# Optimization experiments

Hardware: AMD Instinct MI355X
Metric: run time of the kernel (lower is better)

Reference implementation:

```python
import jax, jax.numpy as jnp
import numpy as np

DIM = 512        # token feature dim
HID = 1024       # expert hidden dim (dim * 2)
E = 16           # num_experts
N = 8192         # num tokens
TOPK = 2         # experts active per token (routing sparsity)


def setup_inputs() -> dict:
    key = jax.random.key(0)
    k_x, k_s, k_w1, k_w2 = jax.random.split(key, 4)
    x = jax.random.normal(k_x, (N, DIM), dtype=jnp.float32)
    # sparse routing scores: top-2 experts per token get nonzero score, rest 0
    scores = jax.random.uniform(k_s, (N, E), dtype=jnp.float32)
    vals, idx = jax.lax.top_k(scores, TOPK)
    routing_tensor = jnp.zeros((N, E), jnp.float32).at[jnp.arange(N)[:, None], idx].set(vals)
    # per-expert MLP params (depth=2, bias=True): Linear(DIM->HID), GELU, Linear(HID->DIM)
    W1 = jax.random.normal(k_w1, (E, DIM, HID), dtype=jnp.float32) * (1.0 / np.sqrt(DIM))
    b1 = jnp.zeros((E, HID), jnp.float32)
    W2 = jax.random.normal(k_w2, (E, HID, DIM), dtype=jnp.float32) * (1.0 / np.sqrt(HID))
    b2 = jnp.zeros((E, DIM), jnp.float32)
    return {"x": x, "routing_tensor": routing_tensor, "W1": W1, "b1": b1, "W2": W2, "b2": b2}


def reference(x, routing_tensor, W1, b1, W2, b2):
    # out[n] = sum_e routing[n,e] * MLP_e(x[n]); rows with score 0 contribute 0,
    # which is exactly the original mask-gather / scatter-add semantics.
    h = jax.nn.gelu(jnp.einsum('nd,edh->enh', x, W1) + b1[:, None, :], approximate=False)
    y = jnp.einsum('enh,ehd->end', h, W2) + b2[:, None, :]  # [E, N, DIM]
    return jnp.einsum('end,ne->nd', y, routing_tensor)       # combine weighted by scores
```

## Files before the change

### kernel.cpp

```cpp
#include <hip/hip_runtime.h>
#include <hip/hip_bf16.h>

#define NTOK 8192
#define DIM 512
#define HID 1024
#define NE 16
#define CAP 1280
#define MT 20

typedef __attribute__((ext_vector_type(8))) short short8;
typedef __attribute__((ext_vector_type(4))) float f32x4;

static __device__ __forceinline__ unsigned short f2bf(float f) {
    __hip_bfloat16 h = __float2bfloat16(f);
    return __builtin_bit_cast(unsigned short, h);
}

static __device__ __forceinline__ void gl_lds16(const unsigned short* g, unsigned short* l) {
    __builtin_amdgcn_global_load_lds(
        (const __attribute__((address_space(1))) unsigned int*)g,
        (__attribute__((address_space(3))) unsigned int*)l, 16, 0, 0);
}

static __device__ __forceinline__ float gelu_f(float v) {
    float u = v * (0.7978845608f + 0.0356774081f * v * v);
    return v / (1.0f + __expf(-2.0f * u));
}

__global__ __launch_bounds__(256) void prep(const float* __restrict__ W1,
                                            const float* __restrict__ W2,
                                            unsigned short* __restrict__ w1t,
                                            unsigned short* __restrict__ w2t,
                                            const float* __restrict__ routing,
                                            int* __restrict__ cnt,
                                            int* __restrict__ sidx,
                                            float* __restrict__ wtb) {
    int b = blockIdx.x;
    int t = threadIdx.x;
    if (b < 4096) {
        __shared__ float tile[64][65];
        const float* src; unsigned short* dst; int R, C, bx, by;
        if (b < 2048) {
            int e = b >> 7, rem = b & 127; bx = rem & 15; by = rem >> 4;
            R = DIM; C = HID;
            src = W1 + (size_t)e * R * C; dst = w1t + (size_t)e * R * C;
        } else {
            int bb = b - 2048;
            int e = bb >> 7, rem = bb & 127; bx = rem & 7; by = rem >> 3;
            R = HID; C = DIM;
            src = W2 + (size_t)e * R * C; dst = w2t + (size_t)e * R * C;
        }
        int c0 = bx * 64, r0 = by * 64;
        int tx = t & 15, ty = t >> 4;
        #pragma unroll
        for (int i = 0; i < 4; i++) {
            float4 v = *(const float4*)(src + (size_t)(r0 + ty + i * 16) * C + c0 + tx * 4);
            tile[ty + i * 16][tx * 4 + 0] = v.x;
            tile[ty + i * 16][tx * 4 + 1] = v.y;
            tile[ty + i * 16][tx * 4 + 2] = v.z;
            tile[ty + i * 16][tx * 4 + 3] = v.w;
        }
        __syncthreads();
        #pragma unroll
        for (int i = 0; i < 4; i++) {
            int dr = ty + i * 16;
            ushort4 o;
            o.x = f2bf(tile[tx * 4 + 0][dr]);
            o.y = f2bf(tile[tx * 4 + 1][dr]);
            o.z = f2bf(tile[tx * 4 + 2][dr]);
            o.w = f2bf(tile[tx * 4 + 3][dr]);
            *(ushort4*)(dst + (size_t)(c0 + dr) * R + r0 + tx * 4) = o;
        }
    } else {
        __shared__ int lcnt[NE], lbase[NE];
        int n = (b - 4096) * 256 + t;
        if (t < NE) lcnt[t] = 0;
        __syncthreads();
        int mye[2]; float myw[2]; int mypos[2]; int slot = 0;
        #pragma unroll
        for (int e = 0; e < NE; e++) {
            float r = routing[n * NE + e];
            if (r != 0.0f && slot < 2) {
                mye[slot] = e; myw[slot] = r;
                mypos[slot] = atomicAdd(&lcnt[e], 1);
                slot++;
            }
        }
        __syncthreads();
        if (t < NE) lbase[t] = atomicAdd(&cnt[t], lcnt[t]);
        __syncthreads();
        for (int s = 0; s < slot; s++) {
            int e = mye[s];
            int p = lbase[e] + mypos[s];
            if (p < CAP) { sidx[e * CAP + p] = n * 2 + s; wtb[e * CAP + p] = myw[s]; }
        }
    }
}

__global__ void gather_x(const float* __restrict__ x, const int* __restrict__ cnt,
                         const int* __restrict__ sidx, unsigned short* __restrict__ xg) {
    int b = blockIdx.x;
    int e = b / CAP, row = b - e * CAP;
    int t = threadIdx.x;
    int c = cnt[e]; c = c > CAP ? CAP : c;
    ushort4 o;
    if (row < c) {
        int n = sidx[b] >> 1;
        float4 v = ((const float4*)(x + (size_t)n * DIM))[t];
        o.x = f2bf(v.x); o.y = f2bf(v.y); o.z = f2bf(v.z); o.w = f2bf(v.w);
    } else {
        o.x = 0; o.y = 0; o.z = 0; o.w = 0;
    }
    ((ushort4*)(xg + (size_t)b * DIM))[t] = o;
}

template <int K>
__device__ __forceinline__ void mfma_main64(const unsigned short* __restrict__ A,
                                            const unsigned short* __restrict__ B,
                                            unsigned short* As, unsigned short* Bs,
                                            f32x4 acc[2][4]) {
    int t = threadIdx.x;
    int wave = t >> 6, lane = t & 63;
    int wm = wave >> 1, wn = wave & 1;
    int quad = lane >> 4, l16 = lane & 15;
    int lr = lane >> 3;
    int col = (lane & 7) << 3;
    for (int kc = 0; kc < K; kc += 64) {
        __syncthreads();
        #pragma unroll
        for (int j = 0; j < 2; j++) {
            int rb = wave * 16 + j * 8;
            gl_lds16(A + (size_t)(rb + lr) * K + kc + col, As + rb * 64);
        }
        #pragma unroll
        for (int j = 0; j < 4; j++) {
            int rb = wave * 32 + j * 8;
            gl_lds16(B + (size_t)(rb + lr) * K + kc + col, Bs + rb * 64);
        }
        __syncthreads();
        #pragma unroll
        for (int kk = 0; kk < 64; kk += 32) {
            short8 av[2], bv[4];
            #pragma unroll
            for (int mt = 0; mt < 2; mt++)
                av[mt] = *(const short8*)(&As[(wm * 32 + mt * 16 + l16) * 64 + kk + quad * 8]);
            #pragma unroll
            for (int nt = 0; nt < 4; nt++)
                bv[nt] = *(const short8*)(&Bs[(wn * 64 + nt * 16 + l16) * 64 + kk + quad * 8]);
            #pragma unroll
            for (int mt = 0; mt < 2; mt++)
                #pragma unroll
                for (int nt = 0; nt < 4; nt++)
                    acc[mt][nt] = __builtin_amdgcn_mfma_f32_16x16x32_bf16(
                        av[mt], bv[nt], acc[mt][nt], 0, 0, 0);
        }
    }
}


__global__ __launch_bounds__(256, 5) void gemm1_gelu(
    const unsigned short* __restrict__ xg, const unsigned short* __restrict__ w1t,
    const float* __restrict__ b1, const int* __restrict__ cnt,
    unsigned short* __restrict__ hbuf) {
    __shared__ __align__(16) unsigned short As[64 * 64];
    __shared__ __align__(16) unsigned short Bs[128 * 64];
    int L = blockIdx.x;
    int cc = L & 7, n = (L >> 3) & 7, g = L >> 6;
    int pi = cc + (g << 3);
    int e = pi / MT, m = pi % MT;
    int c = cnt[e]; c = c > CAP ? CAP : c;
    int m0 = m * 64;
    if (m0 >= c) return;
    int n0 = n * 128;
    const unsigned short* A = xg + ((size_t)e * CAP + m0) * DIM;
    const unsigned short* B = w1t + ((size_t)e * HID + n0) * DIM;
    f32x4 z = {0.f, 0.f, 0.f, 0.f};
    f32x4 acc[2][4];
    #pragma unroll
    for (int mt = 0; mt < 2; mt++)
        #pragma unroll
        for (int nt = 0; nt < 4; nt++) acc[mt][nt] = z;
    mfma_main64<DIM>(A, B, As, Bs, acc);
    int t = threadIdx.x;
    int wave = t >> 6, lane = t & 63;
    int wm = wave >> 1, wn = wave & 1, quad = lane >> 4, l16 = lane & 15;
    #pragma unroll
    for (int nt = 0; nt < 4; nt++) {
        int gn = n0 + wn * 64 + nt * 16 + l16;
        float bias = b1[e * HID + gn];
        #pragma unroll
        for (int mt = 0; mt < 2; mt++) {
            #pragma unroll
            for (int r = 0; r < 4; r++) {
                int gm = m0 + wm * 32 + mt * 16 + quad * 4 + r;
                float v = acc[mt][nt][r] + bias;
                hbuf[((size_t)e * CAP + gm) * HID + gn] = f2bf(gelu_f(v));
            }
        }
    }
}

__global__ __launch_bounds__(256, 5) void gemm2_store(
    const unsigned short* __restrict__ hbuf, const unsigned short* __restrict__ w2t,
    const float* __restrict__ b2, const int* __restrict__ cnt,
    const int* __restrict__ sidx, const float* __restrict__ wtb,
    float* __restrict__ ybuf) {
    __shared__ __align__(16) unsigned short As[64 * 64];
    __shared__ __align__(16) unsigned short Bs[128 * 64];
    int L = blockIdx.x;
    int cc = L & 7, n = (L >> 3) & 3, g = L >> 5;
    int pi = cc + (g << 3);
    int e = pi / MT, m = pi % MT;
    int c = cnt[e]; c = c > CAP ? CAP : c;
    int m0 = m * 64;
    if (m0 >= c) return;
    int n0 = n * 128;
    const unsigned short* A = hbuf + ((size_t)e * CAP + m0) * HID;
    const unsigned short* B = w2t + ((size_t)e * DIM + n0) * HID;
    f32x4 z = {0.f, 0.f, 0.f, 0.f};
    f32x4 acc[2][4];
    #pragma unroll
    for (int mt = 0; mt < 2; mt++)
        #pragma unroll
        for (int nt = 0; nt < 4; nt++) acc[mt][nt] = z;
    mfma_main64<HID>(A, B, As, Bs, acc);
    int t = threadIdx.x;
    int wave = t >> 6, lane = t & 63;
    int wm = wave >> 1, wn = wave & 1, quad = lane >> 4, l16 = lane & 15;
    #pragma unroll
    for (int mt = 0; mt < 2; mt++) {
        #pragma unroll
        for (int r = 0; r < 4; r++) {
            int gm = m0 + wm * 32 + mt * 16 + quad * 4 + r;
            if (gm < c) {
                int si = sidx[e * CAP + gm];
                float wgt = wtb[e * CAP + gm];
                float* yrow = ybuf + (size_t)si * DIM;
                #pragma unroll
                for (int nt = 0; nt < 4; nt++) {
                    int gn = n0 + wn * 64 + nt * 16 + l16;
                    yrow[gn] = wgt * (acc[mt][nt][r] + b2[e * DIM + gn]);
                }
            }
        }
    }
}

__global__ void combine(const float* __restrict__ yb, float* __restrict__ out) {
    int i = blockIdx.x * 256 + threadIdx.x;
    int n = i >> 7, d4 = i & 127;
    float4 a = ((const float4*)(yb + (size_t)(2 * n) * DIM))[d4];
    float4 b = ((const float4*)(yb + (size_t)(2 * n + 1) * DIM))[d4];
    float4 o;
    o.x = a.x + b.x; o.y = a.y + b.y; o.z = a.z + b.z; o.w = a.w + b.w;
    ((float4*)(out + (size_t)n * DIM))[d4] = o;
}

extern "C" void kernel_launch(void* const* d_in, const int* in_sizes, int n_in,
                              void* d_out, int out_size, void* d_ws, size_t ws_size,
                              hipStream_t stream) {
    const float* x       = (const float*)d_in[0];
    const float* routing = (const float*)d_in[1];
    const float* W1      = (const float*)d_in[2];
    const float* b1      = (const float*)d_in[3];
    const float* W2      = (const float*)d_in[4];
    const float* b2      = (const float*)d_in[5];
    float* out = (float*)d_out;

    char* w = (char*)d_ws;
    int*   cnt  = (int*)w;
    int*   sidx = (int*)(w + 256);
    float* wtb  = (float*)(w + 256 + NE * CAP * 4);
    char* base = w + 256 + NE * CAP * 8;
    unsigned short* xg  = (unsigned short*)base;
    unsigned short* hb  = xg + (size_t)NE * CAP * DIM;
    unsigned short* w1t = hb + (size_t)NE * CAP * HID;
    unsigned short* w2t = w1t + (size_t)NE * HID * DIM;
    float* ybuf = (float*)(w2t + (size_t)NE * DIM * HID);

    hipMemsetAsync(cnt, 0, 256, stream);

    prep<<<4096 + NTOK / 256, 256, 0, stream>>>(W1, W2, w1t, w2t, routing, cnt, sidx, wtb);
    gather_x<<<NE * CAP, 128, 0, stream>>>(x, cnt, sidx, xg);

    gemm1_gelu<<<8 * MT * NE, 256, 0, stream>>>(xg, w1t, b1, cnt, hb);
    gemm2_store<<<4 * MT * NE, 256, 0, stream>>>(hb, w2t, b2, cnt, sidx, wtb, ybuf);
    combine<<<(NTOK * DIM / 4) / 256, 256, 0, stream>>>(ybuf, out);
}
```

Measured before the change: 224.2 us.

## Fuse token gather and bf16 conversion into gemm1 A-tile load; widen transpose stores

Drops the separate gather_x kernel and its bf16 xg buffer. gemm1 now reads routed token rows of x directly through sidx, converts them to bf16 in registers and writes them to LDS. The weight transpose also now stores 8 bf16 values per thread instead of 4. This saves a kernel launch and a full write and read of the gathered activations. In exchange, each of the 8 N-tile blocks re-reads and re-converts the fp32 rows, and the synchronous A-tile loads may stall the MFMA loop.

Measured after the change: 253.7 us. 13.2% more time.

```diff
diff --git a/kernel.cpp b/kernel.cpp
--- a/kernel.cpp
+++ b/kernel.cpp
@@ -9,6 +9,7 @@
 #define MT 20
 
 typedef __attribute__((ext_vector_type(8))) short short8;
+typedef __attribute__((ext_vector_type(8))) unsigned short us8;
 typedef __attribute__((ext_vector_type(4))) float f32x4;
 
 static __device__ __forceinline__ unsigned short f2bf(float f) {
@@ -61,15 +62,15 @@
             tile[ty + i * 16][tx * 4 + 3] = v.w;
         }
         __syncthreads();
-        #pragma unroll
-        for (int i = 0; i < 4; i++) {
-            int dr = ty + i * 16;
-            ushort4 o;
-            o.x = f2bf(tile[tx * 4 + 0][dr]);
-            o.y = f2bf(tile[tx * 4 + 1][dr]);
-            o.z = f2bf(tile[tx * 4 + 2][dr]);
-            o.w = f2bf(tile[tx * 4 + 3][dr]);
-            *(ushort4*)(dst + (size_t)(c0 + dr) * R + r0 + tx * 4) = o;
+        int seg = t & 7;
+        #pragma unroll
+        for (int i = 0; i < 2; i++) {
+            int dr = (t >> 3) + i * 32;
+            us8 o;
+            #pragma unroll
+            for (int j = 0; j < 8; j++)
+                o[j] = f2bf(tile[seg * 8 + j][dr]);
+            *(us8*)(dst + (size_t)(c0 + dr) * R + r0 + seg * 8) = o;
         }
     } else {
         __shared__ int lcnt[NE], lbase[NE];
@@ -97,21 +98,93 @@
     }
 }
 
-__global__ void gather_x(const float* __restrict__ x, const int* __restrict__ cnt,
-                         const int* __restrict__ sidx, unsigned short* __restrict__ xg) {
-    int b = blockIdx.x;
-    int e = b / CAP, row = b - e * CAP;
+
+__global__ __launch_bounds__(256, 5) void gemm1_gelu(
+    const float* __restrict__ x, const unsigned short* __restrict__ w1t,
+    const float* __restrict__ b1, const int* __restrict__ cnt,
+    const int* __restrict__ sidx, unsigned short* __restrict__ hbuf) {
+    __shared__ __align__(16) unsigned short As[64 * 64];
+    __shared__ __align__(16) unsigned short Bs[128 * 64];
+    int L = blockIdx.x;
+    int cc = L & 7, n = (L >> 3) & 7, g = L >> 6;
+    int pi = cc + (g << 3);
+    int e = pi / MT, m = pi % MT;
+    int c = cnt[e]; c = c > CAP ? CAP : c;
+    int m0 = m * 64;
+    if (m0 >= c) return;
+    int n0 = n * 128;
+    const unsigned short* B = w1t + ((size_t)e * HID + n0) * DIM;
+
     int t = threadIdx.x;
-    int c = cnt[e]; c = c > CAP ? CAP : c;
-    ushort4 o;
-    if (row < c) {
-        int n = sidx[b] >> 1;
-        float4 v = ((const float4*)(x + (size_t)n * DIM))[t];
-        o.x = f2bf(v.x); o.y = f2bf(v.y); o.z = f2bf(v.z); o.w = f2bf(v.w);
-    } else {
-        o.x = 0; o.y = 0; o.z = 0; o.w = 0;
-    }
-    ((ushort4*)(xg + (size_t)b * DIM))[t] = o;
+    int wave = t >> 6, lane = t & 63;
+    int wm = wave >> 1, wn = wave & 1;
+    int quad = lane >> 4, l16 = lane & 15;
+    int lr = lane >> 3;
+    int colB = (lane & 7) << 3;
+
+    int rA = t >> 4, cA = (t & 15) * 4;
+    const float* xrow[4];
+    #pragma unroll
+    for (int p = 0; p < 4; p++) {
+        int gr = m0 + rA + p * 16;
+        int si = (gr < c) ? sidx[e * CAP + gr] : -1;
+        xrow[p] = (si >= 0) ? (x + (size_t)(si >> 1) * DIM) : nullptr;
+    }
+
+    f32x4 z = {0.f, 0.f, 0.f, 0.f};
+    f32x4 acc[2][4];
+    #pragma unroll
+    for (int mt = 0; mt < 2; mt++)
+        #pragma unroll
+        for (int nt = 0; nt < 4; nt++) acc[mt][nt] = z;
+
+    for (int kc = 0; kc < DIM; kc += 64) {
+        __syncthreads();
+        #pragma unroll
+        for (int j = 0; j < 4; j++) {
+            int rb = wave * 32 + j * 8;
+            gl_lds16(B + (size_t)(rb + lr) * DIM + kc + colB, Bs + rb * 64);
+        }
+        #pragma unroll
+        for (int p = 0; p < 4; p++) {
+            float4 v = xrow[p] ? *(const float4*)(xrow[p] + kc + cA)
+                               : make_float4(0.f, 0.f, 0.f, 0.f);
+            ushort4 o;
+            o.x = f2bf(v.x); o.y = f2bf(v.y); o.z = f2bf(v.z); o.w = f2bf(v.w);
+            *(ushort4*)(&As[(rA + p * 16) * 64 + cA]) = o;
+        }
+        __syncthreads();
+        #pragma unroll
+        for (int kk = 0; kk < 64; kk += 32) {
+            short8 av[2], bv[4];
+            #pragma unroll
+            for (int mt = 0; mt < 2; mt++)
+                av[mt] = *(const short8*)(&As[(wm * 32 + mt * 16 + l16) * 64 + kk + quad * 8]);
+            #pragma unroll
+            for (int nt = 0; nt < 4; nt++)
+                bv[nt] = *(const short8*)(&Bs[(wn * 64 + nt * 16 + l16) * 64 + kk + quad * 8]);
+            #pragma unroll
+            for (int mt = 0; mt < 2; mt++)
+                #pragma unroll
+                for (int nt = 0; nt < 4; nt++)
+                    acc[mt][nt] = __builtin_amdgcn_mfma_f32_16x16x32_bf16(
+                        av[mt], bv[nt], acc[mt][nt], 0, 0, 0);
+        }
+    }
+    #pragma unroll
+    for (int nt = 0; nt < 4; nt++) {
+        int gn = n0 + wn * 64 + nt * 16 + l16;
+        float bias = b1[e * HID + gn];
+        #pragma unroll
+        for (int mt = 0; mt < 2; mt++) {
+            #pragma unroll
+            for (int r = 0; r < 4; r++) {
+                int gm = m0 + wm * 32 + mt * 16 + quad * 4 + r;
+                float v = acc[mt][nt][r] + bias;
+                hbuf[((size_t)e * CAP + gm) * HID + gn] = f2bf(gelu_f(v));
+            }
+        }
+    }
 }
 
 template <int K>
@@ -153,49 +226,6 @@
                 for (int nt = 0; nt < 4; nt++)
                     acc[mt][nt] = __builtin_amdgcn_mfma_f32_16x16x32_bf16(
                         av[mt], bv[nt], acc[mt][nt], 0, 0, 0);
-        }
-    }
-}
-
-
-__global__ __launch_bounds__(256, 5) void gemm1_gelu(
-    const unsigned short* __restrict__ xg, const unsigned short* __restrict__ w1t,
-    const float* __restrict__ b1, const int* __restrict__ cnt,
-    unsigned short* __restrict__ hbuf) {
-    __shared__ __align__(16) unsigned short As[64 * 64];
-    __shared__ __align__(16) unsigned short Bs[128 * 64];
-    int L = blockIdx.x;
-    int cc = L & 7, n = (L >> 3) & 7, g = L >> 6;
-    int pi = cc + (g << 3);
-    int e = pi / MT, m = pi % MT;
-    int c = cnt[e]; c = c > CAP ? CAP : c;
-    int m0 = m * 64;
-    if (m0 >= c) return;
-    int n0 = n * 128;
-    const unsigned short* A = xg + ((size_t)e * CAP + m0) * DIM;
-    const unsigned short* B = w1t + ((size_t)e * HID + n0) * DIM;
-    f32x4 z = {0.f, 0.f, 0.f, 0.f};
-    f32x4 acc[2][4];
-    #pragma unroll
-    for (int mt = 0; mt < 2; mt++)
-        #pragma unroll
-        for (int nt = 0; nt < 4; nt++) acc[mt][nt] = z;
-    mfma_main64<DIM>(A, B, As, Bs, acc);
-    int t = threadIdx.x;
-    int wave = t >> 6, lane = t & 63;
-    int wm = wave >> 1, wn = wave & 1, quad = lane >> 4, l16 = lane & 15;
-    #pragma unroll
-    for (int nt = 0; nt < 4; nt++) {
-        int gn = n0 + wn * 64 + nt * 16 + l16;
-        float bias = b1[e * HID + gn];
-        #pragma unroll
-        for (int mt = 0; mt < 2; mt++) {
-            #pragma unroll
-            for (int r = 0; r < 4; r++) {
-                int gm = m0 + wm * 32 + mt * 16 + quad * 4 + r;
-                float v = acc[mt][nt][r] + bias;
-                hbuf[((size_t)e * CAP + gm) * HID + gn] = f2bf(gelu_f(v));
-            }
         }
     }
 }
@@ -272,8 +302,7 @@
     int*   sidx = (int*)(w + 256);
     float* wtb  = (float*)(w + 256 + NE * CAP * 4);
     char* base = w + 256 + NE * CAP * 8;
-    unsigned short* xg  = (unsigned short*)base;
-    unsigned short* hb  = xg + (size_t)NE * CAP * DIM;
+    unsigned short* hb  = (unsigned short*)base;
     unsigned short* w1t = hb + (size_t)NE * CAP * HID;
     unsigned short* w2t = w1t + (size_t)NE * HID * DIM;
     float* ybuf = (float*)(w2t + (size_t)NE * DIM * HID);
@@ -281,9 +310,8 @@
     hipMemsetAsync(cnt, 0, 256, stream);
 
     prep<<<4096 + NTOK / 256, 256, 0, stream>>>(W1, W2, w1t, w2t, routing, cnt, sidx, wtb);
-    gather_x<<<NE * CAP, 128, 0, stream>>>(x, cnt, sidx, xg);
-
-    gemm1_gelu<<<8 * MT * NE, 256, 0, stream>>>(xg, w1t, b1, cnt, hb);
+
+    gemm1_gelu<<<8 * MT * NE, 256, 0, stream>>>(x, w1t, b1, cnt, sidx, hb);
     gemm2_store<<<4 * MT * NE, 256, 0, stream>>>(hb, w2t, b2, cnt, sidx, wtb, ybuf);
     combine<<<(NTOK * DIM / 4) / 256, 256, 0, stream>>>(ybuf, out);
 }
```

## Split routing into own kernel and fuse x gather into weight-transpose kernel

Applied to the files above, without the earlier changes.

Routing/counting moves into a small standalone kernel, and the x gather/bf16 conversion is merged into the weight transpose kernel as extra blocks. Each gather block now handles four rows with 16-byte stores, and the transpose writes 8 bf16 values per store instead of 4. The goal is to cut the tiny 128-thread gather blocks, let the gather overlap with the weight conversion, and widen global stores. It adds a launch for the routing kernel, and the transpose now reads LDS with a different access pattern.

Result: no change. 223.0 us (-0.5%).

```diff
diff --git a/kernel.cpp b/kernel.cpp
--- a/kernel.cpp
+++ b/kernel.cpp
@@ -9,6 +9,7 @@
 #define MT 20
 
 typedef __attribute__((ext_vector_type(8))) short short8;
+typedef __attribute__((ext_vector_type(8))) unsigned short us8;
 typedef __attribute__((ext_vector_type(4))) float f32x4;
 
 static __device__ __forceinline__ unsigned short f2bf(float f) {
@@ -27,14 +28,43 @@
     return v / (1.0f + __expf(-2.0f * u));
 }
 
-__global__ __launch_bounds__(256) void prep(const float* __restrict__ W1,
-                                            const float* __restrict__ W2,
-                                            unsigned short* __restrict__ w1t,
-                                            unsigned short* __restrict__ w2t,
-                                            const float* __restrict__ routing,
-                                            int* __restrict__ cnt,
-                                            int* __restrict__ sidx,
-                                            float* __restrict__ wtb) {
+__global__ __launch_bounds__(256) void route_fill(const float* __restrict__ routing,
+                                                  int* __restrict__ cnt,
+                                                  int* __restrict__ sidx,
+                                                  float* __restrict__ wtb) {
+    __shared__ int lcnt[NE], lbase[NE];
+    int t = threadIdx.x;
+    int n = blockIdx.x * 256 + t;
+    if (t < NE) lcnt[t] = 0;
+    __syncthreads();
+    int mye[2]; float myw[2]; int mypos[2]; int slot = 0;
+    #pragma unroll
+    for (int e = 0; e < NE; e++) {
+        float r = routing[n * NE + e];
+        if (r != 0.0f && slot < 2) {
+            mye[slot] = e; myw[slot] = r;
+            mypos[slot] = atomicAdd(&lcnt[e], 1);
+            slot++;
+        }
+    }
+    __syncthreads();
+    if (t < NE) lbase[t] = atomicAdd(&cnt[t], lcnt[t]);
+    __syncthreads();
+    for (int s = 0; s < slot; s++) {
+        int e = mye[s];
+        int p = lbase[e] + mypos[s];
+        if (p < CAP) { sidx[e * CAP + p] = n * 2 + s; wtb[e * CAP + p] = myw[s]; }
+    }
+}
+
+__global__ __launch_bounds__(256) void prep2(const float* __restrict__ W1,
+                                             const float* __restrict__ W2,
+                                             unsigned short* __restrict__ w1t,
+                                             unsigned short* __restrict__ w2t,
+                                             const float* __restrict__ x,
+                                             const int* __restrict__ cnt,
+                                             const int* __restrict__ sidx,
+                                             unsigned short* __restrict__ xg) {
     int b = blockIdx.x;
     int t = threadIdx.x;
     if (b < 4096) {
@@ -61,57 +91,36 @@
             tile[ty + i * 16][tx * 4 + 3] = v.w;
         }
         __syncthreads();
-        #pragma unroll
-        for (int i = 0; i < 4; i++) {
-            int dr = ty + i * 16;
-            ushort4 o;
-            o.x = f2bf(tile[tx * 4 + 0][dr]);
-            o.y = f2bf(tile[tx * 4 + 1][dr]);
-            o.z = f2bf(tile[tx * 4 + 2][dr]);
-            o.w = f2bf(tile[tx * 4 + 3][dr]);
-            *(ushort4*)(dst + (size_t)(c0 + dr) * R + r0 + tx * 4) = o;
+        int seg = t & 7;
+        #pragma unroll
+        for (int i = 0; i < 2; i++) {
+            int dr = (t >> 3) + i * 32;
+            us8 o;
+            #pragma unroll
+            for (int j = 0; j < 8; j++)
+                o[j] = f2bf(tile[seg * 8 + j][dr]);
+            *(us8*)(dst + (size_t)(c0 + dr) * R + r0 + seg * 8) = o;
         }
     } else {
-        __shared__ int lcnt[NE], lbase[NE];
-        int n = (b - 4096) * 256 + t;
-        if (t < NE) lcnt[t] = 0;
-        __syncthreads();
-        int mye[2]; float myw[2]; int mypos[2]; int slot = 0;
-        #pragma unroll
-        for (int e = 0; e < NE; e++) {
-            float r = routing[n * NE + e];
-            if (r != 0.0f && slot < 2) {
-                mye[slot] = e; myw[slot] = r;
-                mypos[slot] = atomicAdd(&lcnt[e], 1);
-                slot++;
-            }
-        }
-        __syncthreads();
-        if (t < NE) lbase[t] = atomicAdd(&cnt[t], lcnt[t]);
-        __syncthreads();
-        for (int s = 0; s < slot; s++) {
-            int e = mye[s];
-            int p = lbase[e] + mypos[s];
-            if (p < CAP) { sidx[e * CAP + p] = n * 2 + s; wtb[e * CAP + p] = myw[s]; }
-        }
-    }
-}
-
-__global__ void gather_x(const float* __restrict__ x, const int* __restrict__ cnt,
-                         const int* __restrict__ sidx, unsigned short* __restrict__ xg) {
-    int b = blockIdx.x;
-    int e = b / CAP, row = b - e * CAP;
-    int t = threadIdx.x;
-    int c = cnt[e]; c = c > CAP ? CAP : c;
-    ushort4 o;
-    if (row < c) {
-        int n = sidx[b] >> 1;
-        float4 v = ((const float4*)(x + (size_t)n * DIM))[t];
-        o.x = f2bf(v.x); o.y = f2bf(v.y); o.z = f2bf(v.z); o.w = f2bf(v.w);
-    } else {
-        o.x = 0; o.y = 0; o.z = 0; o.w = 0;
-    }
-    ((ushort4*)(xg + (size_t)b * DIM))[t] = o;
+        int gi = b - 4096;
+        int lane = t & 63, rl = t >> 6;
+        int row = gi * 4 + rl;
+        int e = row / CAP, r = row - e * CAP;
+        int c = cnt[e]; c = c > CAP ? CAP : c;
+        us8 o;
+        if (r < c) {
+            int n = sidx[row] >> 1;
+            const float* xr = x + (size_t)n * DIM + lane * 8;
+            float4 v0 = *(const float4*)xr;
+            float4 v1 = *(const float4*)(xr + 4);
+            o[0] = f2bf(v0.x); o[1] = f2bf(v0.y); o[2] = f2bf(v0.z); o[3] = f2bf(v0.w);
+            o[4] = f2bf(v1.x); o[5] = f2bf(v1.y); o[6] = f2bf(v1.z); o[7] = f2bf(v1.w);
+        } else {
+            #pragma unroll
+            for (int j = 0; j < 8; j++) o[j] = 0;
+        }
+        *(us8*)(xg + (size_t)row * DIM + lane * 8) = o;
+    }
 }
 
 template <int K>
@@ -280,8 +289,8 @@
 
     hipMemsetAsync(cnt, 0, 256, stream);
 
-    prep<<<4096 + NTOK / 256, 256, 0, stream>>>(W1, W2, w1t, w2t, routing, cnt, sidx, wtb);
-    gather_x<<<NE * CAP, 128, 0, stream>>>(x, cnt, sidx, xg);
+    route_fill<<<NTOK / 256, 256, 0, stream>>>(routing, cnt, sidx, wtb);
+    prep2<<<4096 + 5120, 256, 0, stream>>>(W1, W2, w1t, w2t, x, cnt, sidx, xg);
 
     gemm1_gelu<<<8 * MT * NE, 256, 0, stream>>>(xg, w1t, b1, cnt, hb);
     gemm2_store<<<4 * MT * NE, 256, 0, stream>>>(hb, w2t, b2, cnt, sidx, wtb, ybuf);
```
